# Kernel tuning notes

Measured on AMD Instinct MI355X. Metric: run time of the kernel, lower is better.

## Reference

```python
import jax, jax.numpy as jnp
import numpy as np

B, T, I, H = 512, 49, 96, 1024  # batch, input_window_size-1, 3*nbones, hidden


def setup_inputs() -> dict:
    key = jax.random.key(0)
    k1, k2, k3, k4, k5 = jax.random.split(key, 5)
    s = 1.0 / np.sqrt(H)  # torch GRUCell init scale
    return {
        "enc_in": jax.random.normal(k1, (B, T, I), dtype=jnp.float32),
        "W_ih": jax.random.uniform(k2, (3 * H, I), jnp.float32, -s, s),
        "W_hh": jax.random.uniform(k3, (3 * H, H), jnp.float32, -s, s),
        "b_ih": jax.random.uniform(k4, (3 * H,), jnp.float32, -s, s),
        "b_hh": jax.random.uniform(k5, (3 * H,), jnp.float32, -s, s),
        "train": 1,
    }


def reference(enc_in, W_ih, W_hh, b_ih, b_hh, train):
    # Precompute input projections for all timesteps: [T, B, 3H]
    gi = jnp.einsum("bti,gi->tbg", enc_in, W_ih) + b_ih
    hdim = W_hh.shape[1]

    def step(h, gi_t):
        gh = h @ W_hh.T + b_hh                      # [B, 3H]
        ir, iz, inn = jnp.split(gi_t, 3, axis=-1)   # torch gate order: r, z, n
        hr, hz, hn = jnp.split(gh, 3, axis=-1)
        r = jax.nn.sigmoid(ir + hr)
        z = jax.nn.sigmoid(iz + hz)
        n = jnp.tanh(inn + r * hn)
        h_new = (1.0 - z) * n + z * h
        return h_new, None

    h0 = jnp.zeros((enc_in.shape[0], hdim), dtype=enc_in.dtype)
    h_last, _ = jax.lax.scan(step, h0, gi)
    return h_last  # enc_state: [B, H]
```

## Files before the change

kernel.cpp:

```cpp
#include <hip/hip_runtime.h>
#include <hip/hip_bf16.h>

#define B_ 512
#define T_ 49
#define I_ 96
#define H_ 1024
#define NBLK 256
#define NGRP 8
#define GSZ  32

typedef __attribute__((ext_vector_type(4))) float f32x4;
typedef __attribute__((ext_vector_type(8))) short s16x8;

__device__ __forceinline__ unsigned short f2bf(float f) {
    unsigned int u = __float_as_uint(f);
    unsigned int r = (u + 0x7FFFu + ((u >> 16) & 1u)) >> 16;
    return (unsigned short)r;
}
__device__ __forceinline__ float sigmoidf_(float x) {
    return 1.0f / (1.0f + __expf(-x));
}
__device__ __forceinline__ float tanhf_(float x) {
    return 1.0f - 2.0f / (__expf(2.0f * x) + 1.0f);
}

__device__ __forceinline__ void gload_lds16(const unsigned short* g, unsigned short* l) {
    __builtin_amdgcn_global_load_lds(
        (const __attribute__((address_space(1))) void*)g,
        (__attribute__((address_space(3))) void*)l, 16, 0, 0);
}

__global__ void quantize_kernel(const float* __restrict__ Whh,
                                const float* __restrict__ Wih,
                                const float* __restrict__ x,
                                unsigned short* __restrict__ Whh_bf,
                                unsigned short* __restrict__ Wih_bf,
                                unsigned short* __restrict__ xT_bf,
                                unsigned int* __restrict__ bar) {
    const long stride = (long)gridDim.x * blockDim.x;
    const long idx = (long)blockIdx.x * blockDim.x + threadIdx.x;

    if (blockIdx.x == 0)
        for (int i = threadIdx.x; i < T_ * 10 * 64; i += 256) bar[i] = 0;

    const long nWhh4 = (long)3 * H_ * H_ / 4;
    const long nWih4 = (long)3 * H_ * I_ / 4;
    const long nX4   = (long)B_ * T_ * I_ / 4;

    for (long i = idx; i < nWhh4; i += stride) {
        float4 v = ((const float4*)Whh)[i];
        ushort4 o; o.x = f2bf(v.x); o.y = f2bf(v.y); o.z = f2bf(v.z); o.w = f2bf(v.w);
        ((ushort4*)Whh_bf)[i] = o;
    }
    for (long i = idx; i < nWih4; i += stride) {
        float4 v = ((const float4*)Wih)[i];
        ushort4 o; o.x = f2bf(v.x); o.y = f2bf(v.y); o.z = f2bf(v.z); o.w = f2bf(v.w);
        ((ushort4*)Wih_bf)[i] = o;
    }
    for (long i = idx; i < nX4; i += stride) {
        float4 v = ((const float4*)x)[i];
        ushort4 o; o.x = f2bf(v.x); o.y = f2bf(v.y); o.z = f2bf(v.z); o.w = f2bf(v.w);
        const long e = i * 4;
        const int b  = (int)(e / (T_ * I_));
        const int rm = (int)(e - (long)b * (T_ * I_));
        const int tt = rm / I_;
        const int ii = rm - tt * I_;
        ((ushort4*)xT_bf)[(((long)tt * B_ + b) * I_ + ii) >> 2] = o;
    }
}

__global__ __launch_bounds__(512)
void gru_persist3(const unsigned short* __restrict__ Whh_bf,
                  const unsigned short* __restrict__ Wih_bf,
                  const unsigned short* __restrict__ xT_bf,
                  const float* __restrict__ b_ih,
                  const float* __restrict__ b_hh,
                  unsigned short* __restrict__ hbf0,
                  unsigned short* __restrict__ hbf1,
                  float* __restrict__ out,
                  unsigned int* __restrict__ bar)
{
    __shared__ __align__(16) unsigned short Wl[105 * 512];

    const int tid = threadIdx.x;
    const int w   = tid >> 6;
    const int l   = tid & 63;
    const int l15 = l & 15;
    const int l4  = l >> 4;

    const int bid  = blockIdx.x;
    const int xcd  = bid & 7;
    const int r_   = bid >> 3;
    const int blkb = r_ & 3;
    const int blkj = xcd * 8 + (r_ >> 2);
    const int b0   = blkb * 128;
    const int j0   = blkj * 16;
    const int jg   = j0 + l15;
    const int brow = b0 + w * 16;
    const int grp  = bid >> 5;

    for (int p = w; p < 105; p += 8) {
        const unsigned short* src;
        if (p < 96) {
            const int g = p >> 5, ks = p & 31;
            src = Whh_bf + ((long)g * H_ + j0 + l15) * H_ + ks * 32 + l4 * 8;
        } else {
            const int q = p - 96, g = q / 3, ks = q - g * 3;
            src = Wih_bf + ((long)g * H_ + j0 + l15) * I_ + ks * 32 + l4 * 8;
        }
        gload_lds16(src, &Wl[p * 512]);
    }

    const float bR   = b_ih[jg] + b_hh[jg];
    const float bZ   = b_ih[H_ + jg] + b_hh[H_ + jg];
    const float bihN = b_ih[2 * H_ + jg];
    const float bhhN = b_hh[2 * H_ + jg];

    float hreg[4] = {0.f, 0.f, 0.f, 0.f};

    __syncthreads();

    for (int t = 0; t < T_; ++t) {
        const unsigned short* hin  = (t & 1) ? hbf1 : hbf0;
        unsigned short*       hout = (t & 1) ? hbf0 : hbf1;

        f32x4 accR  = (f32x4){0.f, 0.f, 0.f, 0.f};
        f32x4 accZ  = (f32x4){0.f, 0.f, 0.f, 0.f};
        f32x4 accNi = (f32x4){0.f, 0.f, 0.f, 0.f};
        f32x4 accNh = (f32x4){0.f, 0.f, 0.f, 0.f};

        {
            const unsigned short* Ax = xT_bf + ((long)t * B_ + brow + l15) * I_ + l4 * 8;
#pragma unroll
            for (int ks = 0; ks < 3; ++ks) {
                s16x8 a  = *(const s16x8*)(Ax + ks * 32);
                const unsigned short* wt = &Wl[(96 + ks) * 512 + l * 8];
                s16x8 br = *(const s16x8*)(wt);
                s16x8 bz = *(const s16x8*)(wt + 3 * 512);
                s16x8 bn = *(const s16x8*)(wt + 6 * 512);
                accR  = __builtin_amdgcn_mfma_f32_16x16x32_bf16(a, br, accR, 0, 0, 0);
                accZ  = __builtin_amdgcn_mfma_f32_16x16x32_bf16(a, bz, accZ, 0, 0, 0);
                accNi = __builtin_amdgcn_mfma_f32_16x16x32_bf16(a, bn, accNi, 0, 0, 0);
            }
        }

        if (t > 0) {
            const unsigned short* Ab = hin + (long)(brow + l15) * H_ + l4 * 8;
            s16x8 ar[12];
#pragma unroll
            for (int p = 0; p < 12; ++p)
                ar[p] = *(const s16x8*)(Ab + p * 32);
#pragma unroll
            for (int ks = 0; ks < 32; ++ks) {
                const int slot = ks % 12;
                s16x8 a = ar[slot];
                if (ks < 20)
                    ar[slot] = *(const s16x8*)(Ab + (ks + 12) * 32);
                const unsigned short* wt = &Wl[ks * 512 + l * 8];
                s16x8 br = *(const s16x8*)(wt);
                s16x8 bz = *(const s16x8*)(wt + 32 * 512);
                s16x8 bn = *(const s16x8*)(wt + 64 * 512);
                accR  = __builtin_amdgcn_mfma_f32_16x16x32_bf16(a, br, accR, 0, 0, 0);
                accZ  = __builtin_amdgcn_mfma_f32_16x16x32_bf16(a, bz, accZ, 0, 0, 0);
                accNh = __builtin_amdgcn_mfma_f32_16x16x32_bf16(a, bn, accNh, 0, 0, 0);
            }
        }

#pragma unroll
        for (int r = 0; r < 4; ++r) {
            const float rg = sigmoidf_(accR[r] + bR);
            const float zg = sigmoidf_(accZ[r] + bZ);
            const float ng = tanhf_(accNi[r] + bihN + rg * (accNh[r] + bhhN));
            hreg[r] = (1.0f - zg) * ng + zg * hreg[r];
            const long off = (long)(brow + l4 * 4 + r) * H_ + jg;
            if (t < T_ - 1) hout[off] = f2bf(hreg[r]);
            else            out[off]  = hreg[r];
        }

        if (t < T_ - 1) {
            __syncthreads();
            if (tid == 0) {
                unsigned int* gcnt = &bar[(t * 10 + grp) * 64];
                unsigned int* root = &bar[(t * 10 + 8) * 64];
                unsigned int* flag = &bar[(t * 10 + 9) * 64];
                unsigned int old = __hip_atomic_fetch_add(gcnt, 1u, __ATOMIC_RELEASE,
                                                          __HIP_MEMORY_SCOPE_AGENT);
                if (old == GSZ - 1) {
                    unsigned int o2 = __hip_atomic_fetch_add(root, 1u, __ATOMIC_RELAXED,
                                                             __HIP_MEMORY_SCOPE_AGENT);
                    if (o2 == NGRP - 1)
                        __hip_atomic_store(flag, 1u, __ATOMIC_RELEASE,
                                           __HIP_MEMORY_SCOPE_AGENT);
                }
                while (__hip_atomic_load(flag, __ATOMIC_RELAXED,
                                         __HIP_MEMORY_SCOPE_AGENT) == 0)
                    __builtin_amdgcn_s_sleep(4);
                (void)__hip_atomic_load(flag, __ATOMIC_ACQUIRE,
                                        __HIP_MEMORY_SCOPE_AGENT);
            }
            __syncthreads();
        }
    }
}

extern "C" void kernel_launch(void* const* d_in, const int* in_sizes, int n_in,
                              void* d_out, int out_size, void* d_ws, size_t ws_size,
                              hipStream_t stream) {
    const float* enc_in = (const float*)d_in[0];
    const float* W_ih   = (const float*)d_in[1];
    const float* W_hh   = (const float*)d_in[2];
    const float* b_ih   = (const float*)d_in[3];
    const float* b_hh   = (const float*)d_in[4];
    float* out = (float*)d_out;

    char* ws = (char*)d_ws;
    unsigned short* Whh_bf = (unsigned short*)(ws);
    unsigned short* Wih_bf = (unsigned short*)(ws + 6291456);
    unsigned short* xT_bf  = (unsigned short*)(ws + 6881280);
    unsigned short* hbf0   = (unsigned short*)(ws + 11698176);
    unsigned short* hbf1   = (unsigned short*)(ws + 12746752);
    unsigned int*   bar    = (unsigned int*)(ws + 13795328);

    quantize_kernel<<<dim3(1024), dim3(256), 0, stream>>>(W_hh, W_ih, enc_in,
                                                          Whh_bf, Wih_bf, xT_bf, bar);

    void* args[] = {(void*)&Whh_bf, (void*)&Wih_bf, (void*)&xT_bf,
                    (void*)&b_ih, (void*)&b_hh,
                    (void*)&hbf0, (void*)&hbf1, (void*)&out, (void*)&bar};
    hipLaunchCooperativeKernel((const void*)gru_persist3,
                               dim3(256), dim3(512), args, 0, stream);
}
```

Baseline: 817.0 us.

## Partition GRU work per XCD with per-XCD flag barriers instead of global barrier

Each block reads its hardware XCD id and takes a slot in it, so every XCD owns a 64-row batch slice and the 32 blocks on that XCD split the hidden columns. The global two-level atomic barrier is replaced by per-XCD flag arrays: each block sets its own flag after a step, and the next step spins until all 32 flags on its XCD are set. This relies on all h exchange happening within the XCD's L2. The R and Z recurrent weights stay in LDS, while the N-gate weights and W_ih are now streamed from global memory each step. The h loads use relaxed atomics, and the release/acquire ordering is weakened, which risks memory-ordering bugs and assumes exactly 32 blocks land on each XCD.

```diff
diff --git a/kernel.cpp b/kernel.cpp
--- a/kernel.cpp
+++ b/kernel.cpp
@@ -5,9 +5,6 @@
 #define T_ 49
 #define I_ 96
 #define H_ 1024
-#define NBLK 256
-#define NGRP 8
-#define GSZ  32
 
 typedef __attribute__((ext_vector_type(4))) float f32x4;
 typedef __attribute__((ext_vector_type(8))) short s16x8;
@@ -28,6 +25,15 @@
     __builtin_amdgcn_global_load_lds(
         (const __attribute__((address_space(1))) void*)g,
         (__attribute__((address_space(3))) void*)l, 16, 0, 0);
+}
+
+__device__ __forceinline__ s16x8 loadA16(const unsigned short* p) {
+    union { unsigned long long q[2]; s16x8 v; } u;
+    u.q[0] = __hip_atomic_load((const unsigned long long*)p,
+                               __ATOMIC_RELAXED, __HIP_MEMORY_SCOPE_AGENT);
+    u.q[1] = __hip_atomic_load((const unsigned long long*)(p + 4),
+                               __ATOMIC_RELAXED, __HIP_MEMORY_SCOPE_AGENT);
+    return u.v;
 }
 
 __global__ void quantize_kernel(const float* __restrict__ Whh,
@@ -41,7 +47,7 @@
     const long idx = (long)blockIdx.x * blockDim.x + threadIdx.x;
 
     if (blockIdx.x == 0)
-        for (int i = threadIdx.x; i < T_ * 10 * 64; i += 256) bar[i] = 0;
+        for (int i = threadIdx.x; i < (T_ * 8 + 8) * 64; i += 256) bar[i] = 0;
 
     const long nWhh4 = (long)3 * H_ * H_ / 4;
     const long nWih4 = (long)3 * H_ * I_ / 4;
@@ -70,44 +76,54 @@
 }
 
 __global__ __launch_bounds__(512)
-void gru_persist3(const unsigned short* __restrict__ Whh_bf,
-                  const unsigned short* __restrict__ Wih_bf,
-                  const unsigned short* __restrict__ xT_bf,
-                  const float* __restrict__ b_ih,
-                  const float* __restrict__ b_hh,
-                  unsigned short* __restrict__ hbf0,
-                  unsigned short* __restrict__ hbf1,
-                  float* __restrict__ out,
-                  unsigned int* __restrict__ bar)
+void gru_xcd(const unsigned short* __restrict__ Whh_bf,
+             const unsigned short* __restrict__ Wih_bf,
+             const unsigned short* __restrict__ xT_bf,
+             const float* __restrict__ b_ih,
+             const float* __restrict__ b_hh,
+             unsigned short* __restrict__ hbf0,
+             unsigned short* __restrict__ hbf1,
+             float* __restrict__ out,
+             unsigned int* __restrict__ bar)
 {
-    __shared__ __align__(16) unsigned short Wl[105 * 512];
+    __shared__ __align__(16) unsigned short Wl[128 * 512];
+    __shared__ int s_xcd, s_slot;
 
     const int tid = threadIdx.x;
     const int w   = tid >> 6;
     const int l   = tid & 63;
     const int l15 = l & 15;
     const int l4  = l >> 4;
-
-    const int bid  = blockIdx.x;
-    const int xcd  = bid & 7;
-    const int r_   = bid >> 3;
-    const int blkb = r_ & 3;
-    const int blkj = xcd * 8 + (r_ >> 2);
-    const int b0   = blkb * 128;
-    const int j0   = blkj * 16;
-    const int jg   = j0 + l15;
-    const int brow = b0 + w * 16;
-    const int grp  = bid >> 5;
-
-    for (int p = w; p < 105; p += 8) {
-        const unsigned short* src;
-        if (p < 96) {
-            const int g = p >> 5, ks = p & 31;
-            src = Whh_bf + ((long)g * H_ + j0 + l15) * H_ + ks * 32 + l4 * 8;
-        } else {
-            const int q = p - 96, g = q / 3, ks = q - g * 3;
-            src = Wih_bf + ((long)g * H_ + j0 + l15) * I_ + ks * 32 + l4 * 8;
-        }
+    const int mq  = w >> 1;
+    const int nq  = w & 1;
+
+    if (tid == 0) {
+        unsigned int x;
+        asm volatile("s_getreg_b32 %0, hwreg(20, 0, 32)" : "=s"(x));
+        x &= 7;
+        unsigned int sl = __hip_atomic_fetch_add(bar + (T_ * 8) * 64 + x * 64, 1u,
+                                                 __ATOMIC_RELAXED,
+                                                 __HIP_MEMORY_SCOPE_AGENT);
+        s_xcd = (int)x;
+        s_slot = (int)(sl & 31);
+    }
+    __syncthreads();
+    const int xcd  = s_xcd;
+    const int slot = s_slot;
+
+    const int b0   = xcd * 64;
+    const int j0   = slot * 32;
+    const int brow = b0 + mq * 16;
+    const int jg   = j0 + nq * 16 + l15;
+
+#pragma unroll
+    for (int i = 0; i < 16; ++i) {
+        const int p  = w * 16 + i;
+        const int g  = p >> 6;
+        const int jh = (p >> 5) & 1;
+        const int ks = p & 31;
+        const unsigned short* src = Whh_bf
+            + ((long)g * H_ + j0 + jh * 16 + l15) * H_ + ks * 32 + l4 * 8;
         gload_lds16(src, &Wl[p * 512]);
     }
 
@@ -116,9 +132,15 @@
     const float bihN = b_ih[2 * H_ + jg];
     const float bhhN = b_hh[2 * H_ + jg];
 
+    const unsigned short* Vr = Wih_bf + (long)(jg) * I_ + l4 * 8;
+    const unsigned short* Vz = Wih_bf + (long)(H_ + jg) * I_ + l4 * 8;
+    const unsigned short* Vn = Wih_bf + (long)(2 * H_ + jg) * I_ + l4 * 8;
+    const unsigned short* Wnp = Whh_bf + ((long)2 * H_ + jg) * H_ + l4 * 8;
+
+    const unsigned short* WlR = &Wl[(nq * 32) * 512 + l * 8];
+    const unsigned short* WlZ = &Wl[((2 + nq) * 32) * 512 + l * 8];
+
     float hreg[4] = {0.f, 0.f, 0.f, 0.f};
-
-    __syncthreads();
 
     for (int t = 0; t < T_; ++t) {
         const unsigned short* hin  = (t & 1) ? hbf1 : hbf0;
@@ -134,10 +156,9 @@
 #pragma unroll
             for (int ks = 0; ks < 3; ++ks) {
                 s16x8 a  = *(const s16x8*)(Ax + ks * 32);
-                const unsigned short* wt = &Wl[(96 + ks) * 512 + l * 8];
-                s16x8 br = *(const s16x8*)(wt);
-                s16x8 bz = *(const s16x8*)(wt + 3 * 512);
-                s16x8 bn = *(const s16x8*)(wt + 6 * 512);
+                s16x8 br = *(const s16x8*)(Vr + ks * 32);
+                s16x8 bz = *(const s16x8*)(Vz + ks * 32);
+                s16x8 bn = *(const s16x8*)(Vn + ks * 32);
                 accR  = __builtin_amdgcn_mfma_f32_16x16x32_bf16(a, br, accR, 0, 0, 0);
                 accZ  = __builtin_amdgcn_mfma_f32_16x16x32_bf16(a, bz, accZ, 0, 0, 0);
                 accNi = __builtin_amdgcn_mfma_f32_16x16x32_bf16(a, bn, accNi, 0, 0, 0);
@@ -145,21 +166,31 @@
         }
 
         if (t > 0) {
+            const unsigned int* fl = bar + ((long)(t - 1) * 8 + xcd) * 64 + (l & 31);
+            for (;;) {
+                unsigned int f = __hip_atomic_load(fl, __ATOMIC_RELAXED,
+                                                   __HIP_MEMORY_SCOPE_AGENT);
+                if (__all(f != 0)) break;
+                __builtin_amdgcn_s_sleep(1);
+            }
+            asm volatile("" ::: "memory");
+
             const unsigned short* Ab = hin + (long)(brow + l15) * H_ + l4 * 8;
-            s16x8 ar[12];
-#pragma unroll
-            for (int p = 0; p < 12; ++p)
-                ar[p] = *(const s16x8*)(Ab + p * 32);
+
+            s16x8 ar[8], wn[4];
+#pragma unroll
+            for (int p = 0; p < 8; ++p) ar[p] = loadA16(Ab + p * 32);
+#pragma unroll
+            for (int p = 0; p < 4; ++p) wn[p] = *(const s16x8*)(Wnp + p * 32);
+
 #pragma unroll
             for (int ks = 0; ks < 32; ++ks) {
-                const int slot = ks % 12;
-                s16x8 a = ar[slot];
-                if (ks < 20)
-                    ar[slot] = *(const s16x8*)(Ab + (ks + 12) * 32);
-                const unsigned short* wt = &Wl[ks * 512 + l * 8];
-                s16x8 br = *(const s16x8*)(wt);
-                s16x8 bz = *(const s16x8*)(wt + 32 * 512);
-                s16x8 bn = *(const s16x8*)(wt + 64 * 512);
+                s16x8 a  = ar[ks & 7];
+                s16x8 bn = wn[ks & 3];
+                if (ks < 24) ar[ks & 7] = loadA16(Ab + (ks + 8) * 32);
+                if (ks < 28) wn[ks & 3] = *(const s16x8*)(Wnp + (ks + 4) * 32);
+                s16x8 br = *(const s16x8*)(WlR + ks * 512);
+                s16x8 bz = *(const s16x8*)(WlZ + ks * 512);
                 accR  = __builtin_amdgcn_mfma_f32_16x16x32_bf16(a, br, accR, 0, 0, 0);
                 accZ  = __builtin_amdgcn_mfma_f32_16x16x32_bf16(a, bz, accZ, 0, 0, 0);
                 accNh = __builtin_amdgcn_mfma_f32_16x16x32_bf16(a, bn, accNh, 0, 0, 0);
@@ -179,26 +210,9 @@
 
         if (t < T_ - 1) {
             __syncthreads();
-            if (tid == 0) {
-                unsigned int* gcnt = &bar[(t * 10 + grp) * 64];
-                unsigned int* root = &bar[(t * 10 + 8) * 64];
-                unsigned int* flag = &bar[(t * 10 + 9) * 64];
-                unsigned int old = __hip_atomic_fetch_add(gcnt, 1u, __ATOMIC_RELEASE,
-                                                          __HIP_MEMORY_SCOPE_AGENT);
-                if (old == GSZ - 1) {
-                    unsigned int o2 = __hip_atomic_fetch_add(root, 1u, __ATOMIC_RELAXED,
-                                                             __HIP_MEMORY_SCOPE_AGENT);
-                    if (o2 == NGRP - 1)
-                        __hip_atomic_store(flag, 1u, __ATOMIC_RELEASE,
-                                           __HIP_MEMORY_SCOPE_AGENT);
-                }
-                while (__hip_atomic_load(flag, __ATOMIC_RELAXED,
-                                         __HIP_MEMORY_SCOPE_AGENT) == 0)
-                    __builtin_amdgcn_s_sleep(4);
-                (void)__hip_atomic_load(flag, __ATOMIC_ACQUIRE,
-                                        __HIP_MEMORY_SCOPE_AGENT);
-            }
-            __syncthreads();
+            if (tid == 0)
+                __hip_atomic_store(bar + ((long)t * 8 + xcd) * 64 + slot, 1u,
+                                   __ATOMIC_RELAXED, __HIP_MEMORY_SCOPE_AGENT);
         }
     }
 }
@@ -227,6 +241,6 @@
     void* args[] = {(void*)&Whh_bf, (void*)&Wih_bf, (void*)&xT_bf,
                     (void*)&b_ih, (void*)&b_hh,
                     (void*)&hbf0, (void*)&hbf1, (void*)&out, (void*)&bar};
-    hipLaunchCooperativeKernel((const void*)gru_persist3,
+    hipLaunchCooperativeKernel((const void*)gru_xcd,
                                dim3(256), dim3(512), args, 0, stream);
 }
```

After: 1.123 ms. +37.4%, slower.
